# Kernel optimization log

Hardware: AMD Instinct MI355X
Metric: run time of the kernel (lower is better)

## Reference

```python
import jax, jax.numpy as jnp
import numpy as np

B, S, E, H = 2, 2048, 1024, 16
D = E // H  # head dim = 64


def setup_inputs() -> dict:
    key = jax.random.key(0)
    ks = jax.random.split(key, 8)
    return {
        "query": jax.random.normal(ks[0], (B, S, E), dtype=jnp.float32),
        "key": jax.random.normal(ks[1], (B, S, E), dtype=jnp.float32),
        "value": jax.random.normal(ks[2], (B, S, E), dtype=jnp.float32),
        "qkv_weight": jax.random.normal(ks[3], (3 * E, E), dtype=jnp.float32) * 0.02,
        "qkv_bias": jax.random.normal(ks[4], (3 * E,), dtype=jnp.float32) * 0.02,
        "proj_weight": jax.random.normal(ks[5], (E, E), dtype=jnp.float32) * 0.02,
        "proj_bias": jax.random.normal(ks[6], (E,), dtype=jnp.float32) * 0.02,
        "mask": jax.random.normal(ks[7], (S, S), dtype=jnp.float32),
    }


def reference(query, key, value, qkv_weight, qkv_bias, proj_weight, proj_bias, mask):
    # Split fused QKV weight/bias into per-projection chunks ([E,E] each).
    wq, wk, wv = jnp.split(qkv_weight, 3, axis=0)
    bq, bk, bv = jnp.split(qkv_bias, 3, axis=0)

    def proj_heads(x, w, b):
        # [B,S,E] @ [E,E]^T + [E] -> [B,H,S,D]
        y = jnp.einsum("bse,fe->bsf", x, w) + b
        return y.reshape(B, S, H, D).transpose(0, 2, 1, 3)

    q = proj_heads(query, wq, bq)
    k = proj_heads(key, wk, bk)
    v = proj_heads(value, wv, bv)

    scale = 1.0 / jnp.sqrt(jnp.asarray(D, dtype=q.dtype))
    # scores: [B,H,S,S]; mask_type 0 -> additive [S,S] float mask broadcast over B,H
    scores = jnp.einsum("bhsd,bhtd->bhst", q, k) * scale + mask[None, None, :, :]
    attn = jax.nn.softmax(scores, axis=-1)
    ctx = jnp.einsum("bhst,bhtd->bhsd", attn, v)  # [B,H,S,D]
    ctx = ctx.transpose(0, 2, 1, 3).reshape(B, S, E)
    # output projection
    return jnp.einsum("bse,fe->bsf", ctx, proj_weight) + proj_bias
```

## Files before the change

### kernel.cpp

```cpp
#include <hip/hip_runtime.h>
#include <hip/hip_bf16.h>

typedef unsigned short u16;
typedef __attribute__((ext_vector_type(8))) __bf16 bf16x8;
typedef __attribute__((ext_vector_type(4))) __bf16 bf16x4;
typedef __attribute__((ext_vector_type(4))) float f32x4;

#define LOG2E 1.44269504f

#if __has_builtin(__builtin_amdgcn_exp2f)
#define EXP2F(x) __builtin_amdgcn_exp2f(x)
#else
#define EXP2F(x) __expf((x) * 0.69314718f)
#endif

#define GLL16(gptr, lptr) \
  __builtin_amdgcn_global_load_lds((__attribute__((address_space(1))) void*)(gptr), \
                                   (__attribute__((address_space(3))) void*)(lptr), 16, 0, 0)

static __device__ __forceinline__ u16 f2bf(float f) {
  union { float f; unsigned u; } v; v.f = f;
  unsigned r = (v.u + 0x7FFFu + ((v.u >> 16) & 1u)) >> 16;
  return (u16)r;
}

__global__ __launch_bounds__(256) void cvt_f32_bf16(const float* __restrict__ in,
                                                    u16* __restrict__ out, int n4) {
  int i = blockIdx.x * blockDim.x + threadIdx.x;
  if (i < n4) {
    float4 v = ((const float4*)in)[i];
    ushort4 o;
    o.x = f2bf(v.x); o.y = f2bf(v.y); o.z = f2bf(v.z); o.w = f2bf(v.w);
    ((ushort4*)out)[i] = o;
  }
}

__global__ __launch_bounds__(256, 2) void qkv_gemm(
    const u16* __restrict__ xq, const u16* __restrict__ xk, const u16* __restrict__ xv,
    const u16* __restrict__ wbf, const float* __restrict__ bias,
    u16* __restrict__ qout, u16* __restrict__ kout, u16* __restrict__ vtout) {
  __shared__ u16 Al[128 * 32];
  __shared__ u16 Bl[128 * 32];
  const int tid = threadIdx.x;
  const int lane = tid & 63;
  const int w = tid >> 6;
  const int wr = w >> 1, wc = w & 1;
  const int nb = blockIdx.x, mb = blockIdx.y;
  const int row0 = mb * 128;
  const int ncol0 = nb * 128;
  const int which = nb >> 3;
  const u16* A = (which == 0) ? xq : (which == 1) ? xk : xv;
  const u16* Bw = wbf + (size_t)ncol0 * 1024;

  f32x4 acc[4][4];
  f32x4 zero = {0.f, 0.f, 0.f, 0.f};
#pragma unroll
  for (int i = 0; i < 4; i++)
#pragma unroll
    for (int j = 0; j < 4; j++) acc[i][j] = zero;

  const int srow = w * 16 + (lane >> 2);
  const int scol = (lane & 3) * 8;

  for (int k0 = 0; k0 < 1024; k0 += 32) {
#pragma unroll
    for (int p = 0; p < 2; p++) {
      const u16* ga = A + (size_t)(row0 + p * 64 + srow) * 1024 + k0 + scol;
      GLL16(ga, &Al[(p * 64 + w * 16) * 32]);
      const u16* gb = Bw + (size_t)(p * 64 + srow) * 1024 + k0 + scol;
      GLL16(gb, &Bl[(p * 64 + w * 16) * 32]);
    }
    __syncthreads();
    bf16x8 af[4], bfr[4];
#pragma unroll
    for (int mi = 0; mi < 4; mi++)
      af[mi] = *(const bf16x8*)&Al[(wr * 64 + mi * 16 + (lane & 15)) * 32 + (lane >> 4) * 8];
#pragma unroll
    for (int ni = 0; ni < 4; ni++)
      bfr[ni] = *(const bf16x8*)&Bl[(wc * 64 + ni * 16 + (lane & 15)) * 32 + (lane >> 4) * 8];
#pragma unroll
    for (int mi = 0; mi < 4; mi++)
#pragma unroll
      for (int ni = 0; ni < 4; ni++)
        acc[mi][ni] = __builtin_amdgcn_mfma_f32_16x16x32_bf16(af[mi], bfr[ni], acc[mi][ni], 0, 0, 0);
    __syncthreads();
  }

#pragma unroll
  for (int mi = 0; mi < 4; mi++) {
    const int rb = row0 + wr * 64 + mi * 16 + (lane >> 4) * 4;
#pragma unroll
    for (int ni = 0; ni < 4; ni++) {
      const int c = ncol0 + wc * 64 + ni * 16 + (lane & 15);
      const float bs = bias[c];
      const float sc = (which == 0) ? (0.125f * LOG2E) : 1.0f;
      const int fm = c & 1023;
      const int h = fm >> 6, d = fm & 63;
#pragma unroll
      for (int r = 0; r < 4; r++) {
        const int rr = rb + r;
        const int b = rr >> 11, s = rr & 2047;
        const u16 val = f2bf((acc[mi][ni][r] + bs) * sc);
        if (which == 0)
          qout[(((size_t)(b * 16 + h)) * 2048 + s) * 64 + d] = val;
        else if (which == 1)
          kout[(((size_t)(b * 16 + h)) * 2048 + s) * 64 + d] = val;
        else
          vtout[(((size_t)(b * 16 + h)) * 64 + d) * 2048 + s] = val;
      }
    }
  }
}


#define ATTN_TILE(PAR, MC)                                                         \
  {                                                                                \
    f32x4 s0_, s1_, s2_, s3_;                                                      \
    __builtin_amdgcn_s_setprio(1);                                                 \
    {                                                                              \
      bf16x8 a_, b_;                                                               \
      a_ = *(const bf16x8*)(ldsb + Kr0 + 0 + (PAR));                               \
      b_ = *(const bf16x8*)(ldsb + Kr1 + 0 + (PAR));                               \
      s0_ = __builtin_amdgcn_mfma_f32_16x16x32_bf16(a_, q0, MC[0], 0, 0, 0);       \
      s0_ = __builtin_amdgcn_mfma_f32_16x16x32_bf16(b_, q1, s0_, 0, 0, 0);         \
      a_ = *(const bf16x8*)(ldsb + Kr0 + 2048 + (PAR));                            \
      b_ = *(const bf16x8*)(ldsb + Kr1 + 2048 + (PAR));                            \
      s1_ = __builtin_amdgcn_mfma_f32_16x16x32_bf16(a_, q0, MC[1], 0, 0, 0);       \
      s1_ = __builtin_amdgcn_mfma_f32_16x16x32_bf16(b_, q1, s1_, 0, 0, 0);         \
      a_ = *(const bf16x8*)(ldsb + Kr0 + 4096 + (PAR));                            \
      b_ = *(const bf16x8*)(ldsb + Kr1 + 4096 + (PAR));                            \
      s2_ = __builtin_amdgcn_mfma_f32_16x16x32_bf16(a_, q0, MC[2], 0, 0, 0);       \
      s2_ = __builtin_amdgcn_mfma_f32_16x16x32_bf16(b_, q1, s2_, 0, 0, 0);         \
      a_ = *(const bf16x8*)(ldsb + Kr0 + 6144 + (PAR));                            \
      b_ = *(const bf16x8*)(ldsb + Kr1 + 6144 + (PAR));                            \
      s3_ = __builtin_amdgcn_mfma_f32_16x16x32_bf16(a_, q0, MC[3], 0, 0, 0);       \
      s3_ = __builtin_amdgcn_mfma_f32_16x16x32_bf16(b_, q1, s3_, 0, 0, 0);         \
    }                                                                              \
    __builtin_amdgcn_s_setprio(0);                                                 \
    float pm = fmaxf(fmaxf(fmaxf(fmaxf(s0_[0], s0_[1]), fmaxf(s0_[2], s0_[3])),    \
                           fmaxf(fmaxf(s1_[0], s1_[1]), fmaxf(s1_[2], s1_[3]))),   \
                     fmaxf(fmaxf(fmaxf(s2_[0], s2_[1]), fmaxf(s2_[2], s2_[3])),    \
                           fmaxf(fmaxf(s3_[0], s3_[1]), fmaxf(s3_[2], s3_[3]))));  \
                     \
    s0_[0] = EXP2F(s0_[0] - m); s0_[1] = EXP2F(s0_[1] - m);                        \
    s0_[2] = EXP2F(s0_[2] - m); s0_[3] = EXP2F(s0_[3] - m);                        \
    s1_[0] = EXP2F(s1_[0] - m); s1_[1] = EXP2F(s1_[1] - m);                        \
    s1_[2] = EXP2F(s1_[2] - m); s1_[3] = EXP2F(s1_[3] - m);                        \
    s2_[0] = EXP2F(s2_[0] - m); s2_[1] = EXP2F(s2_[1] - m);                        \
    s2_[2] = EXP2F(s2_[2] - m); s2_[3] = EXP2F(s2_[3] - m);                        \
    s3_[0] = EXP2F(s3_[0] - m); s3_[1] = EXP2F(s3_[1] - m);                        \
    s3_[2] = EXP2F(s3_[2] - m); s3_[3] = EXP2F(s3_[3] - m);                        \
    float ps = ((s0_[0] + s0_[1]) + (s0_[2] + s0_[3])) +                           \
               ((s1_[0] + s1_[1]) + (s1_[2] + s1_[3])) +                           \
               ((s2_[0] + s2_[1]) + (s2_[2] + s2_[3])) +                           \
               ((s3_[0] + s3_[1]) + (s3_[2] + s3_[3]));                            \
    pm = fmaxf(pm, __shfl_xor(pm, 16));                                            \
    pm = fmaxf(pm, __shfl_xor(pm, 32));                                            \
    if (__any(pm > m + 8.0f)) {                 \
      const float mn = fmaxf(m, pm);                                               \
      const float al = EXP2F(m - mn);                                              \
      m = mn; lsum *= al; ps *= al;                                                \
      s0_ *= al; s1_ *= al; s2_ *= al; s3_ *= al;                                  \
      ctx[0] *= al; ctx[1] *= al; ctx[2] *= al; ctx[3] *= al;                      \
    }                                                                              \
    lsum += ps;                                                                    \
    {                                                                              \
      bf16x4 p_;                                                                   \
      p_[0] = (__bf16)s0_[0]; p_[1] = (__bf16)s0_[1];                              \
      p_[2] = (__bf16)s0_[2]; p_[3] = (__bf16)s0_[3];                              \
      *(bf16x4*)(ldsb + Pw0) = p_;                                                 \
      p_[0] = (__bf16)s1_[0]; p_[1] = (__bf16)s1_[1];                              \
      p_[2] = (__bf16)s1_[2]; p_[3] = (__bf16)s1_[3];                              \
      *(bf16x4*)(ldsb + Pw1) = p_;                                                 \
      p_[0] = (__bf16)s2_[0]; p_[1] = (__bf16)s2_[1];                              \
      p_[2] = (__bf16)s2_[2]; p_[3] = (__bf16)s2_[3];                              \
      *(bf16x4*)(ldsb + Pw2) = p_;                                                 \
      p_[0] = (__bf16)s3_[0]; p_[1] = (__bf16)s3_[1];                              \
      p_[2] = (__bf16)s3_[2]; p_[3] = (__bf16)s3_[3];                              \
      *(bf16x4*)(ldsb + Pw3) = p_;                                                 \
    }                                                                              \
    {                                                                              \
      bf16x8 pa0 = *(const bf16x8*)(ldsb + Pr0);                                   \
      bf16x8 pa1 = *(const bf16x8*)(ldsb + Pr1);                                   \
      __builtin_amdgcn_s_setprio(1);                                               \
      bf16x8 v0_, v1_;                                                             \
      v0_ = *(const bf16x8*)(ldsb + Kr0 + 16384 + 0 + (PAR));                      \
      v1_ = *(const bf16x8*)(ldsb + Kr1 + 16384 + 0 + (PAR));                      \
      ctx[0] = __builtin_amdgcn_mfma_f32_16x16x32_bf16(v0_, pa0, ctx[0], 0, 0, 0); \
      ctx[0] = __builtin_amdgcn_mfma_f32_16x16x32_bf16(v1_, pa1, ctx[0], 0, 0, 0); \
      v0_ = *(const bf16x8*)(ldsb + Kr0 + 16384 + 2048 + (PAR));                   \
      v1_ = *(const bf16x8*)(ldsb + Kr1 + 16384 + 2048 + (PAR));                   \
      ctx[1] = __builtin_amdgcn_mfma_f32_16x16x32_bf16(v0_, pa0, ctx[1], 0, 0, 0); \
      ctx[1] = __builtin_amdgcn_mfma_f32_16x16x32_bf16(v1_, pa1, ctx[1], 0, 0, 0); \
      v0_ = *(const bf16x8*)(ldsb + Kr0 + 16384 + 4096 + (PAR));                   \
      v1_ = *(const bf16x8*)(ldsb + Kr1 + 16384 + 4096 + (PAR));                   \
      ctx[2] = __builtin_amdgcn_mfma_f32_16x16x32_bf16(v0_, pa0, ctx[2], 0, 0, 0); \
      ctx[2] = __builtin_amdgcn_mfma_f32_16x16x32_bf16(v1_, pa1, ctx[2], 0, 0, 0); \
      v0_ = *(const bf16x8*)(ldsb + Kr0 + 16384 + 6144 + (PAR));                   \
      v1_ = *(const bf16x8*)(ldsb + Kr1 + 16384 + 6144 + (PAR));                   \
      ctx[3] = __builtin_amdgcn_mfma_f32_16x16x32_bf16(v0_, pa0, ctx[3], 0, 0, 0); \
      ctx[3] = __builtin_amdgcn_mfma_f32_16x16x32_bf16(v1_, pa1, ctx[3], 0, 0, 0); \
      __builtin_amdgcn_s_setprio(0);                                               \
    }                                                                              \
  }

__global__ __launch_bounds__(256, 4) void attn_fwd(
    const u16* __restrict__ qbf, const u16* __restrict__ kbf, const u16* __restrict__ vtbf,
    const float* __restrict__ mask, u16* __restrict__ ctxout) {
  __shared__ u16 lds[20480];
  char* ldsb = (char*)lds;
  const int tid = threadIdx.x, lane = tid & 63, w = tid >> 6;
  const int qL = lane & 15, g = lane >> 4;
  const int x = (qL & 7) << 4;
  const int bh = blockIdx.x, qt = blockIdx.y;
  const int qbase = qt * 64;
  const size_t hbase = (size_t)bh * 2048 * 64;
  const int qrow = qbase + w * 16 + qL;

  const int Kr0 = qL * 128 + ((g * 16) ^ x);
  const int Kr1 = qL * 128 + ((g * 16 + 64) ^ x);
  const int Pbase = 32768 + w * 2048;
  const int Pr0 = Pbase + Kr0;
  const int Pr1 = Pbase + Kr1;
  const int Pw0 = Pbase + qL * 128 + (((0 * 32) | (g * 8)) ^ x);
  const int Pw1 = Pbase + qL * 128 + (((1 * 32) | (g * 8)) ^ x);
  const int Pw2 = Pbase + qL * 128 + (((2 * 32) | (g * 8)) ^ x);
  const int Pw3 = Pbase + qL * 128 + (((3 * 32) | (g * 8)) ^ x);
  const int srow = tid >> 3;
  const int scol = (tid & 7) * 8;
  const int S0 = srow * 128 + (((tid & 7) * 16) ^ ((srow & 7) << 4));

  bf16x8 q0 = *(const bf16x8*)&qbf[hbase + (size_t)qrow * 64 + g * 8];
  bf16x8 q1 = *(const bf16x8*)&qbf[hbase + (size_t)qrow * 64 + 32 + g * 8];

  float4 kr0, kr1, vr0, vr1;
  kr0 = *(const float4*)&kbf[hbase + (size_t)srow * 64 + scol];
  kr1 = *(const float4*)&kbf[hbase + (size_t)(32 + srow) * 64 + scol];
  vr0 = *(const float4*)&vtbf[hbase + (size_t)srow * 2048 + scol];
  vr1 = *(const float4*)&vtbf[hbase + (size_t)(32 + srow) * 2048 + scol];
  *(float4*)(ldsb + S0) = kr0;
  *(float4*)(ldsb + S0 + 4096) = kr1;
  *(float4*)(ldsb + S0 + 16384) = vr0;
  *(float4*)(ldsb + S0 + 20480) = vr1;
  kr0 = *(const float4*)&kbf[hbase + (size_t)(64 + srow) * 64 + scol];
  kr1 = *(const float4*)&kbf[hbase + (size_t)(96 + srow) * 64 + scol];
  vr0 = *(const float4*)&vtbf[hbase + (size_t)srow * 2048 + 64 + scol];
  vr1 = *(const float4*)&vtbf[hbase + (size_t)(32 + srow) * 2048 + 64 + scol];

  const u16* kpA = kbf + hbase + (size_t)(128 + srow) * 64 + scol;
  const u16* kpB = kbf + hbase + (size_t)(160 + srow) * 64 + scol;
  const u16* vpA = vtbf + hbase + (size_t)srow * 2048 + 128 + scol;
  const u16* vpB = vtbf + hbase + (size_t)(32 + srow) * 2048 + 128 + scol;
  const float* mp = mask + (size_t)qrow * 2048 + g * 4;

  f32x4 mA[4], mB[4];
#pragma unroll
  for (int tb = 0; tb < 4; tb++)
    mA[tb] = (*(const f32x4*)(mp + tb * 16)) * LOG2E;

  float m = 0.f, lsum = 0.f;
  f32x4 ctx[4];
  f32x4 zero = {0.f, 0.f, 0.f, 0.f};
#pragma unroll
  for (int db = 0; db < 4; db++) ctx[db] = zero;

  __syncthreads();

  for (int i = 0; i < 16; ++i) {
    *(float4*)(ldsb + S0 + 8192) = kr0;
    *(float4*)(ldsb + S0 + 12288) = kr1;
    *(float4*)(ldsb + S0 + 24576) = vr0;
    *(float4*)(ldsb + S0 + 28672) = vr1;
    if (i < 15) {
      kr0 = *(const float4*)kpA;
      kr1 = *(const float4*)kpB;
      vr0 = *(const float4*)vpA;
      vr1 = *(const float4*)vpB;
      kpA += 4096; kpB += 4096; vpA += 64; vpB += 64;
    }
#pragma unroll
    for (int tb = 0; tb < 4; tb++)
      mB[tb] = (*(const f32x4*)(mp + 64 + tb * 16)) * LOG2E;
    ATTN_TILE(0, mA)
    __syncthreads();

    if (i < 15) {
      *(float4*)(ldsb + S0) = kr0;
      *(float4*)(ldsb + S0 + 4096) = kr1;
      *(float4*)(ldsb + S0 + 16384) = vr0;
      *(float4*)(ldsb + S0 + 20480) = vr1;
      kr0 = *(const float4*)kpA;
      kr1 = *(const float4*)kpB;
      vr0 = *(const float4*)vpA;
      vr1 = *(const float4*)vpB;
      kpA += 4096; kpB += 4096; vpA += 64; vpB += 64;
#pragma unroll
      for (int tb = 0; tb < 4; tb++)
        mA[tb] = (*(const f32x4*)(mp + 128 + tb * 16)) * LOG2E;
    }
    ATTN_TILE(8192, mB)
    mp += 128;
    __syncthreads();
  }

  lsum += __shfl_xor(lsum, 16);
  lsum += __shfl_xor(lsum, 32);
  const float inv = 1.0f / lsum;
  const int b = bh >> 4, h = bh & 15;
  u16* orow = ctxout + (size_t)(b * 2048 + qrow) * 1024 + h * 64;
#pragma unroll
  for (int db = 0; db < 4; db++) {
    bf16x4 o;
    o[0] = (__bf16)(ctx[db][0] * inv);
    o[1] = (__bf16)(ctx[db][1] * inv);
    o[2] = (__bf16)(ctx[db][2] * inv);
    o[3] = (__bf16)(ctx[db][3] * inv);
    *(bf16x4*)&orow[db * 16 + g * 4] = o;
  }
}

__global__ __launch_bounds__(256, 2) void proj_gemm(
    const u16* __restrict__ ctx, const u16* __restrict__ wbf,
    const float* __restrict__ bias, float* __restrict__ out) {
  __shared__ u16 Al[128 * 32];
  __shared__ u16 Bl[128 * 32];
  const int tid = threadIdx.x;
  const int lane = tid & 63;
  const int w = tid >> 6;
  const int wr = w >> 1, wc = w & 1;
  const int nb = blockIdx.x, mb = blockIdx.y;
  const int row0 = mb * 128;
  const int ncol0 = nb * 128;
  const u16* Bw = wbf + (size_t)ncol0 * 1024;

  f32x4 acc[4][4];
  f32x4 zero = {0.f, 0.f, 0.f, 0.f};
#pragma unroll
  for (int i = 0; i < 4; i++)
#pragma unroll
    for (int j = 0; j < 4; j++) acc[i][j] = zero;

  const int srow = w * 16 + (lane >> 2);
  const int scol = (lane & 3) * 8;

  for (int k0 = 0; k0 < 1024; k0 += 32) {
#pragma unroll
    for (int p = 0; p < 2; p++) {
      const u16* ga = ctx + (size_t)(row0 + p * 64 + srow) * 1024 + k0 + scol;
      GLL16(ga, &Al[(p * 64 + w * 16) * 32]);
      const u16* gb = Bw + (size_t)(p * 64 + srow) * 1024 + k0 + scol;
      GLL16(gb, &Bl[(p * 64 + w * 16) * 32]);
    }
    __syncthreads();
    bf16x8 af[4], bfr[4];
#pragma unroll
    for (int mi = 0; mi < 4; mi++)
      af[mi] = *(const bf16x8*)&Al[(wr * 64 + mi * 16 + (lane & 15)) * 32 + (lane >> 4) * 8];
#pragma unroll
    for (int ni = 0; ni < 4; ni++)
      bfr[ni] = *(const bf16x8*)&Bl[(wc * 64 + ni * 16 + (lane & 15)) * 32 + (lane >> 4) * 8];
#pragma unroll
    for (int mi = 0; mi < 4; mi++)
#pragma unroll
      for (int ni = 0; ni < 4; ni++)
        acc[mi][ni] = __builtin_amdgcn_mfma_f32_16x16x32_bf16(af[mi], bfr[ni], acc[mi][ni], 0, 0, 0);
    __syncthreads();
  }

#pragma unroll
  for (int mi = 0; mi < 4; mi++) {
    const int rb = row0 + wr * 64 + mi * 16 + (lane >> 4) * 4;
#pragma unroll
    for (int ni = 0; ni < 4; ni++) {
      const int c = ncol0 + wc * 64 + ni * 16 + (lane & 15);
      const float bs = bias[c];
#pragma unroll
      for (int r = 0; r < 4; r++)
        out[(size_t)(rb + r) * 1024 + c] = acc[mi][ni][r] + bs;
    }
  }
}

extern "C" void kernel_launch(void* const* d_in, const int* in_sizes, int n_in,
                              void* d_out, int out_size, void* d_ws, size_t ws_size,
                              hipStream_t stream) {
  const float* query = (const float*)d_in[0];
  const float* key   = (const float*)d_in[1];
  const float* value = (const float*)d_in[2];
  const float* qkvw  = (const float*)d_in[3];
  const float* qkvb  = (const float*)d_in[4];
  const float* projw = (const float*)d_in[5];
  const float* projb = (const float*)d_in[6];
  const float* mask  = (const float*)d_in[7];

  char* ws = (char*)d_ws;
  u16* xq    = (u16*)(ws + 0);
  u16* xk    = (u16*)(ws + 8388608);
  u16* xv    = (u16*)(ws + 16777216);
  u16* wqkv  = (u16*)(ws + 25165824);
  u16* wproj = (u16*)(ws + 31457280);
  u16* qb    = (u16*)(ws + 33554432);
  u16* kb    = (u16*)(ws + 41943040);
  u16* vt    = (u16*)(ws + 50331648);
  u16* cx    = xq;

  cvt_f32_bf16<<<4096, 256, 0, stream>>>(query, xq, 1048576);
  cvt_f32_bf16<<<4096, 256, 0, stream>>>(key, xk, 1048576);
  cvt_f32_bf16<<<4096, 256, 0, stream>>>(value, xv, 1048576);
  cvt_f32_bf16<<<3072, 256, 0, stream>>>(qkvw, wqkv, 786432);
  cvt_f32_bf16<<<1024, 256, 0, stream>>>(projw, wproj, 262144);

  qkv_gemm<<<dim3(24, 32), 256, 0, stream>>>(xq, xk, xv, wqkv, qkvb, qb, kb, vt);
  attn_fwd<<<dim3(32, 32), 256, 0, stream>>>(qb, kb, vt, mask, cx);
  proj_gemm<<<dim3(8, 32), 256, 0, stream>>>(cx, wproj, projb, (float*)d_out);
}
```

Before: 177.8 us.

## Keep softmax probabilities in registers by permuting V staging layout; fuse conversion launches

```diff
diff --git a/kernel.cpp b/kernel.cpp
--- a/kernel.cpp
+++ b/kernel.cpp
@@ -24,15 +24,23 @@
   return (u16)r;
 }
 
-__global__ __launch_bounds__(256) void cvt_f32_bf16(const float* __restrict__ in,
-                                                    u16* __restrict__ out, int n4) {
-  int i = blockIdx.x * blockDim.x + threadIdx.x;
-  if (i < n4) {
-    float4 v = ((const float4*)in)[i];
-    ushort4 o;
-    o.x = f2bf(v.x); o.y = f2bf(v.y); o.z = f2bf(v.z); o.w = f2bf(v.w);
-    ((ushort4*)out)[i] = o;
-  }
+__global__ __launch_bounds__(256) void cvt_all(
+    const float* __restrict__ q, const float* __restrict__ k, const float* __restrict__ v,
+    const float* __restrict__ w1, const float* __restrict__ w2,
+    u16* __restrict__ xq, u16* __restrict__ xk, u16* __restrict__ xv,
+    u16* __restrict__ wq, u16* __restrict__ wp) {
+  const int b = blockIdx.x;
+  const float* src; u16* dst; int off;
+  if (b < 4096)       { src = q;  dst = xq; off = b; }
+  else if (b < 8192)  { src = k;  dst = xk; off = b - 4096; }
+  else if (b < 12288) { src = v;  dst = xv; off = b - 8192; }
+  else if (b < 15360) { src = w1; dst = wq; off = b - 12288; }
+  else                { src = w2; dst = wp; off = b - 15360; }
+  const int i = off * 256 + threadIdx.x;
+  float4 vv = ((const float4*)src)[i];
+  ushort4 o;
+  o.x = f2bf(vv.x); o.y = f2bf(vv.y); o.z = f2bf(vv.z); o.w = f2bf(vv.w);
+  ((ushort4*)dst)[i] = o;
 }
 
 __global__ __launch_bounds__(256, 2) void qkv_gemm(
@@ -112,6 +120,14 @@
   }
 }
 
+
+#define STAGE_KV(KOFF, VOFF)                                        \
+  *(float4*)(ldsb + (KOFF) + S0) = kr0;                             \
+  *(float4*)(ldsb + (KOFF) + 4096 + S0) = kr1;                      \
+  *(float2*)(ldsb + (VOFF) + VS0a) = make_float2(vr0.x, vr0.y);     \
+  *(float2*)(ldsb + (VOFF) + VS0b) = make_float2(vr0.z, vr0.w);     \
+  *(float2*)(ldsb + (VOFF) + VS1a) = make_float2(vr1.x, vr1.y);     \
+  *(float2*)(ldsb + (VOFF) + VS1b) = make_float2(vr1.z, vr1.w);
 
 #define ATTN_TILE(PAR, MC)                                                         \
   {                                                                                \
@@ -164,42 +180,34 @@
       ctx[0] *= al; ctx[1] *= al; ctx[2] *= al; ctx[3] *= al;                      \
     }                                                                              \
     lsum += ps;                                                                    \
+           \
+    bf16x8 pa0, pa1;                                                               \
+    pa0[0] = (__bf16)s0_[0]; pa0[1] = (__bf16)s0_[1];                              \
+    pa0[2] = (__bf16)s0_[2]; pa0[3] = (__bf16)s0_[3];                              \
+    pa0[4] = (__bf16)s1_[0]; pa0[5] = (__bf16)s1_[1];                              \
+    pa0[6] = (__bf16)s1_[2]; pa0[7] = (__bf16)s1_[3];                              \
+    pa1[0] = (__bf16)s2_[0]; pa1[1] = (__bf16)s2_[1];                              \
+    pa1[2] = (__bf16)s2_[2]; pa1[3] = (__bf16)s2_[3];                              \
+    pa1[4] = (__bf16)s3_[0]; pa1[5] = (__bf16)s3_[1];                              \
+    pa1[6] = (__bf16)s3_[2]; pa1[7] = (__bf16)s3_[3];                              \
     {                                                                              \
-      bf16x4 p_;                                                                   \
-      p_[0] = (__bf16)s0_[0]; p_[1] = (__bf16)s0_[1];                              \
-      p_[2] = (__bf16)s0_[2]; p_[3] = (__bf16)s0_[3];                              \
-      *(bf16x4*)(ldsb + Pw0) = p_;                                                 \
-      p_[0] = (__bf16)s1_[0]; p_[1] = (__bf16)s1_[1];                              \
-      p_[2] = (__bf16)s1_[2]; p_[3] = (__bf16)s1_[3];                              \
-      *(bf16x4*)(ldsb + Pw1) = p_;                                                 \
-      p_[0] = (__bf16)s2_[0]; p_[1] = (__bf16)s2_[1];                              \
-      p_[2] = (__bf16)s2_[2]; p_[3] = (__bf16)s2_[3];                              \
-      *(bf16x4*)(ldsb + Pw2) = p_;                                                 \
-      p_[0] = (__bf16)s3_[0]; p_[1] = (__bf16)s3_[1];                              \
-      p_[2] = (__bf16)s3_[2]; p_[3] = (__bf16)s3_[3];                              \
-      *(bf16x4*)(ldsb + Pw3) = p_;                                                 \
-    }                                                                              \
-    {                                                                              \
-      bf16x8 pa0 = *(const bf16x8*)(ldsb + Pr0);                                   \
-      bf16x8 pa1 = *(const bf16x8*)(ldsb + Pr1);                                   \
+      bf16x8 v00 = *(const bf16x8*)(ldsb + Kr0 + 16384 + (PAR));                   \
+      bf16x8 v01 = *(const bf16x8*)(ldsb + Kr1 + 16384 + (PAR));                   \
+      bf16x8 v10 = *(const bf16x8*)(ldsb + Kr0 + 18432 + (PAR));                   \
+      bf16x8 v11 = *(const bf16x8*)(ldsb + Kr1 + 18432 + (PAR));                   \
+      bf16x8 v20 = *(const bf16x8*)(ldsb + Kr0 + 20480 + (PAR));                   \
+      bf16x8 v21 = *(const bf16x8*)(ldsb + Kr1 + 20480 + (PAR));                   \
+      bf16x8 v30 = *(const bf16x8*)(ldsb + Kr0 + 22528 + (PAR));                   \
+      bf16x8 v31 = *(const bf16x8*)(ldsb + Kr1 + 22528 + (PAR));                   \
       __builtin_amdgcn_s_setprio(1);                                               \
-      bf16x8 v0_, v1_;                                                             \
-      v0_ = *(const bf16x8*)(ldsb + Kr0 + 16384 + 0 + (PAR));                      \
-      v1_ = *(const bf16x8*)(ldsb + Kr1 + 16384 + 0 + (PAR));                      \
-      ctx[0] = __builtin_amdgcn_mfma_f32_16x16x32_bf16(v0_, pa0, ctx[0], 0, 0, 0); \
-      ctx[0] = __builtin_amdgcn_mfma_f32_16x16x32_bf16(v1_, pa1, ctx[0], 0, 0, 0); \
-      v0_ = *(const bf16x8*)(ldsb + Kr0 + 16384 + 2048 + (PAR));                   \
-      v1_ = *(const bf16x8*)(ldsb + Kr1 + 16384 + 2048 + (PAR));                   \
-      ctx[1] = __builtin_amdgcn_mfma_f32_16x16x32_bf16(v0_, pa0, ctx[1], 0, 0, 0); \
-      ctx[1] = __builtin_amdgcn_mfma_f32_16x16x32_bf16(v1_, pa1, ctx[1], 0, 0, 0); \
-      v0_ = *(const bf16x8*)(ldsb + Kr0 + 16384 + 4096 + (PAR));                   \
-      v1_ = *(const bf16x8*)(ldsb + Kr1 + 16384 + 4096 + (PAR));                   \
-      ctx[2] = __builtin_amdgcn_mfma_f32_16x16x32_bf16(v0_, pa0, ctx[2], 0, 0, 0); \
-      ctx[2] = __builtin_amdgcn_mfma_f32_16x16x32_bf16(v1_, pa1, ctx[2], 0, 0, 0); \
-      v0_ = *(const bf16x8*)(ldsb + Kr0 + 16384 + 6144 + (PAR));                   \
-      v1_ = *(const bf16x8*)(ldsb + Kr1 + 16384 + 6144 + (PAR));                   \
-      ctx[3] = __builtin_amdgcn_mfma_f32_16x16x32_bf16(v0_, pa0, ctx[3], 0, 0, 0); \
-      ctx[3] = __builtin_amdgcn_mfma_f32_16x16x32_bf16(v1_, pa1, ctx[3], 0, 0, 0); \
+      ctx[0] = __builtin_amdgcn_mfma_f32_16x16x32_bf16(v00, pa0, ctx[0], 0, 0, 0); \
+      ctx[0] = __builtin_amdgcn_mfma_f32_16x16x32_bf16(v01, pa1, ctx[0], 0, 0, 0); \
+      ctx[1] = __builtin_amdgcn_mfma_f32_16x16x32_bf16(v10, pa0, ctx[1], 0, 0, 0); \
+      ctx[1] = __builtin_amdgcn_mfma_f32_16x16x32_bf16(v11, pa1, ctx[1], 0, 0, 0); \
+      ctx[2] = __builtin_amdgcn_mfma_f32_16x16x32_bf16(v20, pa0, ctx[2], 0, 0, 0); \
+      ctx[2] = __builtin_amdgcn_mfma_f32_16x16x32_bf16(v21, pa1, ctx[2], 0, 0, 0); \
+      ctx[3] = __builtin_amdgcn_mfma_f32_16x16x32_bf16(v30, pa0, ctx[3], 0, 0, 0); \
+      ctx[3] = __builtin_amdgcn_mfma_f32_16x16x32_bf16(v31, pa1, ctx[3], 0, 0, 0); \
       __builtin_amdgcn_s_setprio(0);                                               \
     }                                                                              \
   }
@@ -207,7 +215,7 @@
 __global__ __launch_bounds__(256, 4) void attn_fwd(
     const u16* __restrict__ qbf, const u16* __restrict__ kbf, const u16* __restrict__ vtbf,
     const float* __restrict__ mask, u16* __restrict__ ctxout) {
-  __shared__ u16 lds[20480];
+  __shared__ u16 lds[16384];
   char* ldsb = (char*)lds;
   const int tid = threadIdx.x, lane = tid & 63, w = tid >> 6;
   const int qL = lane & 15, g = lane >> 4;
@@ -219,16 +227,17 @@
 
   const int Kr0 = qL * 128 + ((g * 16) ^ x);
   const int Kr1 = qL * 128 + ((g * 16 + 64) ^ x);
-  const int Pbase = 32768 + w * 2048;
-  const int Pr0 = Pbase + Kr0;
-  const int Pr1 = Pbase + Kr1;
-  const int Pw0 = Pbase + qL * 128 + (((0 * 32) | (g * 8)) ^ x);
-  const int Pw1 = Pbase + qL * 128 + (((1 * 32) | (g * 8)) ^ x);
-  const int Pw2 = Pbase + qL * 128 + (((2 * 32) | (g * 8)) ^ x);
-  const int Pw3 = Pbase + qL * 128 + (((3 * 32) | (g * 8)) ^ x);
   const int srow = tid >> 3;
   const int scol = (tid & 7) * 8;
   const int S0 = srow * 128 + (((tid & 7) * 16) ^ ((srow & 7) << 4));
+  const int a_ = tid & 7;
+  const int vW1 = ((a_ >> 2) << 6) + (((2 * a_) & 3) << 4) + (((a_ >> 1) & 1) << 3);
+  const int vW2 = ((a_ >> 2) << 6) + (((2 * a_ + 1) & 3) << 4) + (((a_ >> 1) & 1) << 3);
+  const int sxr = (srow & 7) << 4;
+  const int VS0a = srow * 128 + (vW1 ^ sxr);
+  const int VS0b = srow * 128 + (vW2 ^ sxr);
+  const int VS1a = (32 + srow) * 128 + (vW1 ^ sxr);
+  const int VS1b = (32 + srow) * 128 + (vW2 ^ sxr);
 
   bf16x8 q0 = *(const bf16x8*)&qbf[hbase + (size_t)qrow * 64 + g * 8];
   bf16x8 q1 = *(const bf16x8*)&qbf[hbase + (size_t)qrow * 64 + 32 + g * 8];
@@ -238,10 +247,7 @@
   kr1 = *(const float4*)&kbf[hbase + (size_t)(32 + srow) * 64 + scol];
   vr0 = *(const float4*)&vtbf[hbase + (size_t)srow * 2048 + scol];
   vr1 = *(const float4*)&vtbf[hbase + (size_t)(32 + srow) * 2048 + scol];
-  *(float4*)(ldsb + S0) = kr0;
-  *(float4*)(ldsb + S0 + 4096) = kr1;
-  *(float4*)(ldsb + S0 + 16384) = vr0;
-  *(float4*)(ldsb + S0 + 20480) = vr1;
+  STAGE_KV(0, 16384)
   kr0 = *(const float4*)&kbf[hbase + (size_t)(64 + srow) * 64 + scol];
   kr1 = *(const float4*)&kbf[hbase + (size_t)(96 + srow) * 64 + scol];
   vr0 = *(const float4*)&vtbf[hbase + (size_t)srow * 2048 + 64 + scol];
@@ -267,10 +273,7 @@
   __syncthreads();
 
   for (int i = 0; i < 16; ++i) {
-    *(float4*)(ldsb + S0 + 8192) = kr0;
-    *(float4*)(ldsb + S0 + 12288) = kr1;
-    *(float4*)(ldsb + S0 + 24576) = vr0;
-    *(float4*)(ldsb + S0 + 28672) = vr1;
+    STAGE_KV(8192, 24576)
     if (i < 15) {
       kr0 = *(const float4*)kpA;
       kr1 = *(const float4*)kpB;
@@ -285,10 +288,7 @@
     __syncthreads();
 
     if (i < 15) {
-      *(float4*)(ldsb + S0) = kr0;
-      *(float4*)(ldsb + S0 + 4096) = kr1;
-      *(float4*)(ldsb + S0 + 16384) = vr0;
-      *(float4*)(ldsb + S0 + 20480) = vr1;
+      STAGE_KV(0, 16384)
       kr0 = *(const float4*)kpA;
       kr1 = *(const float4*)kpB;
       vr0 = *(const float4*)vpA;
@@ -404,12 +404,7 @@
   u16* vt    = (u16*)(ws + 50331648);
   u16* cx    = xq;
 
-  cvt_f32_bf16<<<4096, 256, 0, stream>>>(query, xq, 1048576);
-  cvt_f32_bf16<<<4096, 256, 0, stream>>>(key, xk, 1048576);
-  cvt_f32_bf16<<<4096, 256, 0, stream>>>(value, xv, 1048576);
-  cvt_f32_bf16<<<3072, 256, 0, stream>>>(qkvw, wqkv, 786432);
-  cvt_f32_bf16<<<1024, 256, 0, stream>>>(projw, wproj, 262144);
-
+  cvt_all<<<16384, 256, 0, stream>>>(query, key, value, qkvw, projw, xq, xk, xv, wqkv, wproj);
   qkv_gemm<<<dim3(24, 32), 256, 0, stream>>>(xq, xk, xv, wqkv, qkvb, qb, kb, vt);
   attn_fwd<<<dim3(32, 32), 256, 0, stream>>>(qb, kb, vt, mask, cx);
   proj_gemm<<<dim3(8, 32), 256, 0, stream>>>(cx, wproj, projb, (float*)d_out);
```

New measurement: 193.5 us. 1.09x slower.
